# Optimization experiments

Hardware: AMD Instinct MI355X
Metric: run time of the kernel (lower is better)

The kernel has to match this reference:

```python
import jax, jax.numpy as jnp
import numpy as np

B, C, H, W = 4, 256, 64, 64
C8 = C // 8


def setup_inputs() -> dict:
    key = jax.random.key(0)
    ks = jax.random.split(key, 8)
    x = jax.random.normal(ks[0], (B, C, H, W), dtype=jnp.float32)
    valid = jax.random.uniform(ks[1], (B, 1, H, W), dtype=jnp.float32)
    # 1x1 conv weights (kernel_size=1 -> plain channel matmul) + biases
    Wq = jax.random.normal(ks[2], (C8, C), dtype=jnp.float32) * 0.05
    bq = jnp.zeros((C8,), dtype=jnp.float32)
    Wk = jax.random.normal(ks[3], (C8, C), dtype=jnp.float32) * 0.05
    bk = jnp.zeros((C8,), dtype=jnp.float32)
    Wv = jax.random.normal(ks[4], (C, C), dtype=jnp.float32) * 0.05
    bv = jnp.zeros((C,), dtype=jnp.float32)
    gamma = jnp.asarray(0.5, dtype=jnp.float32)  # nonzero so attention path matters
    return {"x": x, "valid": valid, "Wq": Wq, "bq": bq, "Wk": Wk, "bk": bk,
            "Wv": Wv, "bv": bv, "gamma": gamma}


def reference(x, valid, Wq, bq, Wk, bk, Wv, bv, gamma):
    b, c, h, w = x.shape
    n = h * w
    xf = x.reshape(b, c, n)                                   # [B,C,N]
    # valid is already at (H,W): nearest interpolate to same size is identity
    v = valid.reshape(b, 1, n)                                # [B,1,N]
    q = jnp.einsum('oc,bcn->bno', Wq, xf) + bq                # [B,N,C//8]
    k = jnp.einsum('oc,bcn->bon', Wk, xf) + bk[None, :, None] # [B,C//8,N]
    energy = jnp.einsum('bno,bom->bnm', q, k)                 # [B,N,N]
    attn = jax.nn.softmax(energy, axis=-1)
    va = attn * v                                             # mask columns
    scale = 1.0 / jnp.sum(va, axis=2, keepdims=True)          # per-row renorm
    sa = va * scale                                           # [B,N,N]
    pv = jnp.einsum('oc,bcn->bon', Wv, xf) + bv[None, :, None]  # [B,C,N]
    out = jnp.einsum('bon,bmn->bom', pv, sa)                  # bmm(V, A^T)
    out = out.reshape(b, c, h, w)
    return gamma * out + x, sa
```

## Files before the change

kernel.cpp:

```cpp
#include <hip/hip_runtime.h>

typedef unsigned short u16;
typedef unsigned int u32;
typedef __attribute__((ext_vector_type(8))) short short8;
typedef __attribute__((ext_vector_type(4))) float f32x4;
typedef __attribute__((ext_vector_type(2))) unsigned int u32x2;
typedef __attribute__((ext_vector_type(4))) unsigned int u32x4;

#define BB 4
#define CC 256
#define NT 4096
#define L2E 1.4426950408889634f

__device__ __forceinline__ float b2f(u16 v) {
    union { u32 u; float f; } c; c.u = ((u32)v) << 16; return c.f;
}
__device__ __forceinline__ u16 f2b(float f) {
    union { float f; u32 u; } c; c.f = f;
    u32 u = c.u;
    return (u16)((u + 0x7fffu + ((u >> 16) & 1u)) >> 16);
}

__global__ __launch_bounds__(256) void kproj(
    const float* __restrict__ x,
    const float* __restrict__ Wq, const float* __restrict__ bq,
    const float* __restrict__ Wk, const float* __restrict__ bk,
    const float* __restrict__ Wv, const float* __restrict__ bv,
    u16* __restrict__ qh, u16* __restrict__ ql,
    u16* __restrict__ kh, u16* __restrict__ kl,
    u16* __restrict__ pvw)
{
    __shared__ __align__(16) float lA[32][68];
    __shared__ __align__(16) float lX[32][68];
    const int mt = blockIdx.x, nt = blockIdx.y, b = blockIdx.z;
    const int t = threadIdx.x;
    const int tx = t & 15, ty = t >> 4;
    const int n0 = nt * 64;

    float acc[4][4];
    #pragma unroll
    for (int i = 0; i < 4; ++i)
        #pragma unroll
        for (int j = 0; j < 4; ++j) acc[i][j] = 0.f;

    const int rA = t >> 2, kqA = (t & 3) * 8;
    const int rgA = mt * 64 + rA;
    const float* wrow;
    if (rgA < 32)      wrow = Wq + rgA * 256;
    else if (rgA < 64) wrow = Wk + (rgA - 32) * 256;
    else               wrow = Wv + (rgA - 64) * 256;
    const int kX = t >> 3, nn8 = (t & 7) * 8;
    const float* xrow = x + ((size_t)(b * CC + kX)) * NT + n0 + nn8;

    for (int k0 = 0; k0 < 256; k0 += 32) {
        f32x4 wa = *(const f32x4*)(wrow + k0 + kqA);
        f32x4 wb = *(const f32x4*)(wrow + k0 + kqA + 4);
        f32x4 xa = *(const f32x4*)(xrow + (size_t)k0 * NT);
        f32x4 xb = *(const f32x4*)(xrow + (size_t)k0 * NT + 4);
        __syncthreads();
        #pragma unroll
        for (int j = 0; j < 4; ++j) {
            lA[kqA + j    ][rA] = wa[j];
            lA[kqA + j + 4][rA] = wb[j];
        }
        *(f32x4*)&lX[kX][nn8]     = xa;
        *(f32x4*)&lX[kX][nn8 + 4] = xb;
        __syncthreads();
        #pragma unroll
        for (int k = 0; k < 32; ++k) {
            f32x4 av  = *(const f32x4*)&lA[k][ty * 4];
            f32x4 xvv = *(const f32x4*)&lX[k][tx * 4];
            #pragma unroll
            for (int i = 0; i < 4; ++i)
                #pragma unroll
                for (int j = 0; j < 4; ++j)
                    acc[i][j] = fmaf(av[i], xvv[j], acc[i][j]);
        }
    }

    #pragma unroll
    for (int i = 0; i < 4; ++i) {
        const int rg = mt * 64 + ty * 4 + i;
        float bias;
        if (rg < 32)      bias = bq[rg];
        else if (rg < 64) bias = bk[rg - 32];
        else              bias = bv[rg - 64];
        #pragma unroll
        for (int j = 0; j < 4; ++j) {
            const int n = n0 + tx * 4 + j;
            const float val = acc[i][j] + bias;
            const u16 h = f2b(val);
            const u16 l = f2b(val - b2f(h));
            if (rg < 32) {
                const size_t idx = ((size_t)(b * NT + n)) * 32 + rg;
                qh[idx] = h; ql[idx] = l;
            } else if (rg < 64) {
                const size_t idx = ((size_t)(b * NT + n)) * 32 + (rg - 32);
                kh[idx] = h; kl[idx] = l;
            } else {
                pvw[((size_t)b * CC + (rg - 64)) * NT + n] = f2b(val);
            }
        }
    }
}

#define FSTEP(S, CBH, CBL, CV4, NBH, NBL, NV4)                                 \
  {                                                                            \
    const int s_ = (S);                                                        \
    short8 pa00 = *(const short8*)(pva + (size_t)s_ * 64);                     \
    short8 pa01 = *(const short8*)(pva + (size_t)s_ * 64 + 32);                \
    short8 pa10 = *(const short8*)(pva + (size_t)16 * NT + (size_t)s_ * 64);   \
    short8 pa11 = *(const short8*)(pva + (size_t)16 * NT + (size_t)s_ * 64 + 32);\
    if (s_ + 1 < 64) {                                                         \
      const int ct_ = (s_ + 1) * 4 + cq;                                       \
      NBH = *(const short8*)(kh + kbase + (size_t)ct_ * 512);                  \
      NBL = *(const short8*)(kl + kbase + (size_t)ct_ * 512);                  \
      NV4 = *(const f32x4*)(vbase + ct_ * 16 + quad * 4);                      \
    }                                                                          \
    f32x4 d = __builtin_amdgcn_mfma_f32_16x16x32_bf16(CBH, aqh, zero, 0, 0, 0);\
    d = __builtin_amdgcn_mfma_f32_16x16x32_bf16(CBH, aql, d, 0, 0, 0);         \
    d = __builtin_amdgcn_mfma_f32_16x16x32_bf16(CBL, aqh, d, 0, 0, 0);         \
    f32x4 val;                                                                 \
    _Pragma("unroll")                                                          \
    for (int i = 0; i < 4; ++i)                                                \
      val[i] = CV4[i] * exp2f(fminf(d[i], 60.f) * L2E) * inv;                  \
    *(f32x4*)(sap + (size_t)s_ * 64 + cq * 16 + quad * 4) = val;               \
    u32x2 pk;                                                                  \
    pk[0] = (u32)f2b(val[0]) | ((u32)f2b(val[1]) << 16);                       \
    pk[1] = (u32)f2b(val[2]) | ((u32)f2b(val[3]) << 16);                       \
    *(u32x2*)(lwp + (s_ & 1) * 4096) = pk;                                     \
    asm volatile("s_waitcnt lgkmcnt(0)" ::: "memory");                         \
    __builtin_amdgcn_sched_barrier(0);                                         \
    __builtin_amdgcn_s_barrier();                                              \
    __builtin_amdgcn_sched_barrier(0);                                         \
    const char* lb_ = lrp + (s_ & 1) * 4096;                                   \
    _Pragma("unroll")                                                          \
    for (int half = 0; half < 2; ++half) {                                     \
      const int kby_ = ((half * 64 + quad * 16) ^ swz);                        \
      short8 b0 = *(const short8*)(lb_ + l16 * 128 + kby_);                    \
      short8 b1 = *(const short8*)(lb_ + (16 + l16) * 128 + kby_);             \
      short8 a0 = half ? pa01 : pa00;                                          \
      short8 a1 = half ? pa11 : pa10;                                          \
      acc00 = __builtin_amdgcn_mfma_f32_16x16x32_bf16(a0, b0, acc00, 0, 0, 0); \
      acc01 = __builtin_amdgcn_mfma_f32_16x16x32_bf16(a0, b1, acc01, 0, 0, 0); \
      acc10 = __builtin_amdgcn_mfma_f32_16x16x32_bf16(a1, b0, acc10, 0, 0, 0); \
      acc11 = __builtin_amdgcn_mfma_f32_16x16x32_bf16(a1, b1, acc11, 0, 0, 0); \
    }                                                                          \
  }

__global__ __launch_bounds__(512, 4) void ksaout(
    const u16* __restrict__ qh, const u16* __restrict__ ql,
    const u16* __restrict__ kh, const u16* __restrict__ kl,
    const float* __restrict__ valid, const u16* __restrict__ pvw,
    const float* __restrict__ x, const float* __restrict__ gamma,
    float* __restrict__ sa, float* __restrict__ outp)
{
    __shared__ __align__(16) u16 lB[2][32][64];
    __shared__ float sred[2][4][16];
    const int b    = blockIdx.y;
    const int m0   = blockIdx.x * 32;
    const int t    = threadIdx.x;
    const int lane = t & 63;
    const int wv   = t >> 6;
    const int quad = lane >> 4, l16 = lane & 15;
    const int rg   = wv >> 2, cq = wv & 3;
    const int swz  = (l16 & 7) << 4;

    const size_t qbase = ((size_t)(b * NT + m0 + rg * 16 + l16)) * 32 + quad * 8;
    const short8 aqh = *(const short8*)(qh + qbase);
    const short8 aql = *(const short8*)(ql + qbase);
    const size_t kbase = (size_t)b * NT * 32 + (size_t)l16 * 32 + quad * 8;
    const float* vbase = valid + (size_t)b * NT;
    const f32x4 zero = {0.f, 0.f, 0.f, 0.f};

    float sacc = 0.f;
    {
        short8 nbh = *(const short8*)(kh + kbase + (size_t)(cq * 64) * 512);
        short8 nbl = *(const short8*)(kl + kbase + (size_t)(cq * 64) * 512);
        f32x4  nv4 = *(const f32x4*)(vbase + (cq * 64) * 16 + quad * 4);
        for (int s = 0; s < 64; ++s) {
            short8 bh = nbh, bl = nbl;
            f32x4 v4 = nv4;
            if (s + 1 < 64) {
                const int ct = cq * 64 + s + 1;
                nbh = *(const short8*)(kh + kbase + (size_t)ct * 512);
                nbl = *(const short8*)(kl + kbase + (size_t)ct * 512);
                nv4 = *(const f32x4*)(vbase + ct * 16 + quad * 4);
            }
            f32x4 d = __builtin_amdgcn_mfma_f32_16x16x32_bf16(bh, aqh, zero, 0, 0, 0);
            d = __builtin_amdgcn_mfma_f32_16x16x32_bf16(bh, aql, d, 0, 0, 0);
            d = __builtin_amdgcn_mfma_f32_16x16x32_bf16(bl, aqh, d, 0, 0, 0);
            #pragma unroll
            for (int i = 0; i < 4; ++i)
                sacc += v4[i] * exp2f(fminf(d[i], 60.f) * L2E);
        }
    }
    sacc += __shfl_xor(sacc, 16, 64);
    sacc += __shfl_xor(sacc, 32, 64);
    if (lane < 16) sred[rg][cq][l16] = sacc;
    __syncthreads();
    const float inv = 1.0f / (sred[rg][0][l16] + sred[rg][1][l16] +
                              sred[rg][2][l16] + sred[rg][3][l16]);

    const u16* pva = pvw + ((size_t)(b * CC + wv * 32 + l16)) * NT + quad * 8;
    float* sap = sa + ((size_t)(b * NT + m0 + rg * 16 + l16)) * NT;
    char* lwp = (char*)&lB[0][0][0] + (rg * 16 + l16) * 128
              + ((cq * 32 + quad * 8) ^ swz);
    const char* lrp = (const char*)&lB[0][0][0];

    f32x4 acc00 = {0,0,0,0}, acc01 = {0,0,0,0}, acc10 = {0,0,0,0}, acc11 = {0,0,0,0};

    short8 cbh = *(const short8*)(kh + kbase + (size_t)cq * 512);
    short8 cbl = *(const short8*)(kl + kbase + (size_t)cq * 512);
    f32x4  cv4 = *(const f32x4*)(vbase + cq * 16 + quad * 4);
    short8 nbh, nbl; f32x4 nv4;

    for (int s = 0; s < 64; s += 2) {
        FSTEP(s,     cbh, cbl, cv4, nbh, nbl, nv4)
        FSTEP(s + 1, nbh, nbl, nv4, cbh, cbl, cv4)
    }

    const float g = gamma[0];
    #pragma unroll
    for (int ai = 0; ai < 2; ++ai) {
        #pragma unroll
        for (int bi = 0; bi < 2; ++bi) {
            f32x4 acc = (ai == 0) ? ((bi == 0) ? acc00 : acc01)
                                  : ((bi == 0) ? acc10 : acc11);
            #pragma unroll
            for (int i = 0; i < 4; ++i) {
                const int c = wv * 32 + ai * 16 + quad * 4 + i;
                const int m = m0 + bi * 16 + l16;
                const size_t idx = ((size_t)(b * CC + c)) * NT + m;
                outp[idx] = g * acc[i] + x[idx];
            }
        }
    }
}

extern "C" void kernel_launch(void* const* d_in, const int* in_sizes, int n_in,
                              void* d_out, int out_size, void* d_ws, size_t ws_size,
                              hipStream_t stream)
{
    const float* x     = (const float*)d_in[0];
    const float* valid = (const float*)d_in[1];
    const float* Wq    = (const float*)d_in[2];
    const float* bq    = (const float*)d_in[3];
    const float* Wk    = (const float*)d_in[4];
    const float* bk    = (const float*)d_in[5];
    const float* Wv    = (const float*)d_in[6];
    const float* bv    = (const float*)d_in[7];
    const float* gamma = (const float*)d_in[8];

    float* outp = (float*)d_out;
    float* sa   = outp + (size_t)BB * CC * NT;

    u16* qh  = (u16*)d_ws;
    u16* ql  = qh + (size_t)BB * NT * 32;
    u16* kh  = ql + (size_t)BB * NT * 32;
    u16* kl  = kh + (size_t)BB * NT * 32;
    u16* pvw = kl + (size_t)BB * NT * 32;

    kproj<<<dim3(5, 64, BB), 256, 0, stream>>>(x, Wq, bq, Wk, bk, Wv, bv,
                                               qh, ql, kh, kl, pvw);
    ksaout<<<dim3(128, BB), 512, 0, stream>>>(qh, ql, kh, kl, valid, pvw,
                                              x, gamma, sa, outp);
}
```

Before: 531.4 us.

## Software-pipeline attention: triple-buffer LDS and compute P one phase ahead of PV

Restructures the second pass of the fused attention kernel. Each barrier phase now covers two 64-wide key slices, with a 128-wide LDS tile and three rotating buffers. The softmax probabilities for the next phase are computed and written before the PV MFMAs for the current phase run. PV operand loads are prefetched a phase ahead, and the MFMA block is raised in priority with s_setprio. The aim is to halve the number of barriers and overlap the exp/store work with the matrix multiplies, at the cost of more registers (eight prefetched A fragments) and more LDS.

```diff
diff --git a/kernel.cpp b/kernel.cpp
--- a/kernel.cpp
+++ b/kernel.cpp
@@ -104,49 +104,7 @@
     }
 }
 
-#define FSTEP(S, CBH, CBL, CV4, NBH, NBL, NV4)                                 \
-  {                                                                            \
-    const int s_ = (S);                                                        \
-    short8 pa00 = *(const short8*)(pva + (size_t)s_ * 64);                     \
-    short8 pa01 = *(const short8*)(pva + (size_t)s_ * 64 + 32);                \
-    short8 pa10 = *(const short8*)(pva + (size_t)16 * NT + (size_t)s_ * 64);   \
-    short8 pa11 = *(const short8*)(pva + (size_t)16 * NT + (size_t)s_ * 64 + 32);\
-    if (s_ + 1 < 64) {                                                         \
-      const int ct_ = (s_ + 1) * 4 + cq;                                       \
-      NBH = *(const short8*)(kh + kbase + (size_t)ct_ * 512);                  \
-      NBL = *(const short8*)(kl + kbase + (size_t)ct_ * 512);                  \
-      NV4 = *(const f32x4*)(vbase + ct_ * 16 + quad * 4);                      \
-    }                                                                          \
-    f32x4 d = __builtin_amdgcn_mfma_f32_16x16x32_bf16(CBH, aqh, zero, 0, 0, 0);\
-    d = __builtin_amdgcn_mfma_f32_16x16x32_bf16(CBH, aql, d, 0, 0, 0);         \
-    d = __builtin_amdgcn_mfma_f32_16x16x32_bf16(CBL, aqh, d, 0, 0, 0);         \
-    f32x4 val;                                                                 \
-    _Pragma("unroll")                                                          \
-    for (int i = 0; i < 4; ++i)                                                \
-      val[i] = CV4[i] * exp2f(fminf(d[i], 60.f) * L2E) * inv;                  \
-    *(f32x4*)(sap + (size_t)s_ * 64 + cq * 16 + quad * 4) = val;               \
-    u32x2 pk;                                                                  \
-    pk[0] = (u32)f2b(val[0]) | ((u32)f2b(val[1]) << 16);                       \
-    pk[1] = (u32)f2b(val[2]) | ((u32)f2b(val[3]) << 16);                       \
-    *(u32x2*)(lwp + (s_ & 1) * 4096) = pk;                                     \
-    asm volatile("s_waitcnt lgkmcnt(0)" ::: "memory");                         \
-    __builtin_amdgcn_sched_barrier(0);                                         \
-    __builtin_amdgcn_s_barrier();                                              \
-    __builtin_amdgcn_sched_barrier(0);                                         \
-    const char* lb_ = lrp + (s_ & 1) * 4096;                                   \
-    _Pragma("unroll")                                                          \
-    for (int half = 0; half < 2; ++half) {                                     \
-      const int kby_ = ((half * 64 + quad * 16) ^ swz);                        \
-      short8 b0 = *(const short8*)(lb_ + l16 * 128 + kby_);                    \
-      short8 b1 = *(const short8*)(lb_ + (16 + l16) * 128 + kby_);             \
-      short8 a0 = half ? pa01 : pa00;                                          \
-      short8 a1 = half ? pa11 : pa10;                                          \
-      acc00 = __builtin_amdgcn_mfma_f32_16x16x32_bf16(a0, b0, acc00, 0, 0, 0); \
-      acc01 = __builtin_amdgcn_mfma_f32_16x16x32_bf16(a0, b1, acc01, 0, 0, 0); \
-      acc10 = __builtin_amdgcn_mfma_f32_16x16x32_bf16(a1, b0, acc10, 0, 0, 0); \
-      acc11 = __builtin_amdgcn_mfma_f32_16x16x32_bf16(a1, b1, acc11, 0, 0, 0); \
-    }                                                                          \
-  }
+#define MFMA_BF16(A, B, C) __builtin_amdgcn_mfma_f32_16x16x32_bf16(A, B, C, 0, 0, 0)
 
 __global__ __launch_bounds__(512, 4) void ksaout(
     const u16* __restrict__ qh, const u16* __restrict__ ql,
@@ -155,7 +113,7 @@
     const float* __restrict__ x, const float* __restrict__ gamma,
     float* __restrict__ sa, float* __restrict__ outp)
 {
-    __shared__ __align__(16) u16 lB[2][32][64];
+    __shared__ __align__(16) u16 lB[3][32][128];
     __shared__ float sred[2][4][16];
     const int b    = blockIdx.y;
     const int m0   = blockIdx.x * 32;
@@ -187,9 +145,9 @@
                 nbl = *(const short8*)(kl + kbase + (size_t)ct * 512);
                 nv4 = *(const f32x4*)(vbase + ct * 16 + quad * 4);
             }
-            f32x4 d = __builtin_amdgcn_mfma_f32_16x16x32_bf16(bh, aqh, zero, 0, 0, 0);
-            d = __builtin_amdgcn_mfma_f32_16x16x32_bf16(bh, aql, d, 0, 0, 0);
-            d = __builtin_amdgcn_mfma_f32_16x16x32_bf16(bl, aqh, d, 0, 0, 0);
+            f32x4 d = MFMA_BF16(bh, aqh, zero);
+            d = MFMA_BF16(bh, aql, d);
+            d = MFMA_BF16(bl, aqh, d);
             #pragma unroll
             for (int i = 0; i < 4; ++i)
                 sacc += v4[i] * exp2f(fminf(d[i], 60.f) * L2E);
@@ -204,21 +162,89 @@
 
     const u16* pva = pvw + ((size_t)(b * CC + wv * 32 + l16)) * NT + quad * 8;
     float* sap = sa + ((size_t)(b * NT + m0 + rg * 16 + l16)) * NT;
-    char* lwp = (char*)&lB[0][0][0] + (rg * 16 + l16) * 128
-              + ((cq * 32 + quad * 8) ^ swz);
-    const char* lrp = (const char*)&lB[0][0][0];
+    char* lbB = (char*)&lB[0][0][0];
+    const int lwoff = (rg * 16 + l16) * 256 + ((cq * 32 + quad * 8) ^ swz);
 
     f32x4 acc00 = {0,0,0,0}, acc01 = {0,0,0,0}, acc10 = {0,0,0,0}, acc11 = {0,0,0,0};
 
-    short8 cbh = *(const short8*)(kh + kbase + (size_t)cq * 512);
-    short8 cbl = *(const short8*)(kl + kbase + (size_t)cq * 512);
-    f32x4  cv4 = *(const f32x4*)(vbase + cq * 16 + quad * 4);
-    short8 nbh, nbl; f32x4 nv4;
-
-    for (int s = 0; s < 64; s += 2) {
-        FSTEP(s,     cbh, cbl, cv4, nbh, nbl, nv4)
-        FSTEP(s + 1, nbh, nbl, nv4, cbh, cbl, cv4)
-    }
+#define LOADQK(S, BH, BL, VV)                                                  \
+    { int ct_ = (S) * 4 + cq; if (ct_ > 255) ct_ = 255;                        \
+      BH = *(const short8*)(kh + kbase + (size_t)ct_ * 512);                   \
+      BL = *(const short8*)(kl + kbase + (size_t)ct_ * 512);                   \
+      VV = *(const f32x4*)(vbase + ct_ * 16 + quad * 4); }
+
+#define ASTEP(S, J, BUF, BH, BL, VV)                                           \
+    { f32x4 d = MFMA_BF16(BH, aqh, zero);                                      \
+      d = MFMA_BF16(BH, aql, d);                                               \
+      d = MFMA_BF16(BL, aqh, d);                                               \
+      f32x4 val;                                                               \
+      _Pragma("unroll")                                                        \
+      for (int i = 0; i < 4; ++i)                                              \
+          val[i] = VV[i] * exp2f(fminf(d[i], 60.f) * L2E) * inv;               \
+      *(f32x4*)(sap + (size_t)(S) * 64 + cq * 16 + quad * 4) = val;            \
+      u32x2 pk;                                                                \
+      pk[0] = (u32)f2b(val[0]) | ((u32)f2b(val[1]) << 16);                     \
+      pk[1] = (u32)f2b(val[2]) | ((u32)f2b(val[3]) << 16);                     \
+      *(u32x2*)(lbB + (BUF) * 8192 + lwoff + (J) * 128) = pk; }
+
+    short8 qbh0, qbl0, qbh1, qbl1;
+    f32x4 qv0, qv1;
+    short8 pac[8];
+
+    LOADQK(0, qbh0, qbl0, qv0);
+    LOADQK(1, qbh1, qbl1, qv1);
+    ASTEP(0, 0, 0, qbh0, qbl0, qv0);
+    ASTEP(1, 1, 0, qbh1, qbl1, qv1);
+    LOADQK(2, qbh0, qbl0, qv0);
+    LOADQK(3, qbh1, qbl1, qv1);
+    #pragma unroll
+    for (int k4 = 0; k4 < 4; ++k4) {
+        pac[k4]     = *(const short8*)(pva + k4 * 32);
+        pac[4 + k4] = *(const short8*)(pva + (size_t)16 * NT + k4 * 32);
+    }
+    asm volatile("s_waitcnt lgkmcnt(0)" ::: "memory");
+    __builtin_amdgcn_sched_barrier(0);
+    __builtin_amdgcn_s_barrier();
+    __builtin_amdgcn_sched_barrier(0);
+
+    for (int p = 0; p < 32; ++p) {
+        const int rbuf = p % 3;
+        if (p < 31) {
+            const int wbuf = (p + 1) % 3;
+            ASTEP(2 * p + 2, 0, wbuf, qbh0, qbl0, qv0);
+            ASTEP(2 * p + 3, 1, wbuf, qbh1, qbl1, qv1);
+            if (p < 30) {
+                LOADQK(2 * p + 4, qbh0, qbl0, qv0);
+                LOADQK(2 * p + 5, qbh1, qbl1, qv1);
+            }
+            asm volatile("s_waitcnt lgkmcnt(0)" ::: "memory");
+            __builtin_amdgcn_sched_barrier(0);
+            __builtin_amdgcn_s_barrier();
+            __builtin_amdgcn_sched_barrier(0);
+        }
+        __builtin_amdgcn_s_setprio(1);
+        #pragma unroll
+        for (int k4 = 0; k4 < 4; ++k4) {
+            const int kby = ((k4 * 64 + quad * 16) ^ swz);
+            short8 b0 = *(const short8*)(lbB + rbuf * 8192 + l16 * 256 + kby);
+            short8 b1 = *(const short8*)(lbB + rbuf * 8192 + (16 + l16) * 256 + kby);
+            acc00 = MFMA_BF16(pac[k4], b0, acc00);
+            acc01 = MFMA_BF16(pac[k4], b1, acc01);
+            acc10 = MFMA_BF16(pac[4 + k4], b0, acc10);
+            acc11 = MFMA_BF16(pac[4 + k4], b1, acc11);
+        }
+        __builtin_amdgcn_s_setprio(0);
+        if (p < 31) {
+            #pragma unroll
+            for (int k4 = 0; k4 < 4; ++k4) {
+                pac[k4]     = *(const short8*)(pva + (size_t)(p + 1) * 128 + k4 * 32);
+                pac[4 + k4] = *(const short8*)(pva + (size_t)(p + 1) * 128
+                                               + (size_t)16 * NT + k4 * 32);
+            }
+        }
+    }
+#undef LOADQK
+#undef ASTEP
 
     const float g = gamma[0];
     #pragma unroll
```

Result: no change. 522.8 us (-1.6%).
